# Performance work log

Hardware: AMD Instinct MI355X
Metric: run time of the kernel (lower is better)

## Reference

```python
import jax, jax.numpy as jnp
import numpy as np

D_MODEL = 1024
NUM_HEADS = 16
HEAD_DIM = D_MODEL // NUM_HEADS


def setup_inputs() -> dict:
    key = jax.random.key(0)
    ks = jax.random.split(key, 9)
    s = 1.0 / np.sqrt(D_MODEL)
    inp = {"x": jax.random.normal(ks[0], (2, 2048, D_MODEL), dtype=jnp.float32)}
    for i, name in enumerate(["q", "k", "v", "o"]):
        inp[f"W_{name}"] = jax.random.uniform(ks[1 + i], (D_MODEL, D_MODEL), dtype=jnp.float32, minval=-s, maxval=s)
        inp[f"b_{name}"] = jax.random.uniform(ks[5 + i], (D_MODEL,), dtype=jnp.float32, minval=-s, maxval=s)
    return inp


def reference(x, W_q, b_q, W_k, b_k, W_v, b_v, W_o, b_o):
    B, S, _ = x.shape
    def split_heads(t):  # [B,S,D] -> [B,H,S,Dh]
        return t.reshape(B, S, NUM_HEADS, HEAD_DIM).transpose(0, 2, 1, 3)
    q = split_heads(x @ W_q.T + b_q)
    k = split_heads(x @ W_k.T + b_k)
    v = split_heads(x @ W_v.T + b_v)
    scale = 1.0 / np.sqrt(HEAD_DIM).astype(np.float32)
    scores = jnp.einsum('bhqd,bhkd->bhqk', q, k) * scale  # [B,H,S,S]
    attn = jax.nn.softmax(scores, axis=-1)
    out = jnp.einsum('bhqk,bhkd->bhqd', attn, v)  # [B,H,S,Dh]
    out = out.transpose(0, 2, 1, 3).reshape(B, S, D_MODEL)
    return out @ W_o.T + b_o
```

## Files before the change

### kernel.cpp

```cpp
#include <hip/hip_runtime.h>
#include <hip/hip_bf16.h>

typedef __attribute__((ext_vector_type(8))) short short8;
typedef __attribute__((ext_vector_type(4))) float f32x4;
typedef __attribute__((ext_vector_type(16))) float f32x16;
typedef unsigned short ushort_t;
typedef unsigned int uint_t;

#define LOG2E 1.4426950408889634f

#if __has_builtin(__builtin_amdgcn_exp2f)
#define EXP2(x) __builtin_amdgcn_exp2f(x)
#else
#define EXP2(x) exp2f(x)
#endif

__device__ __forceinline__ ushort_t f2bf(float f) {
    union { float f; unsigned int i; } x; x.f = f;
    unsigned int r = x.i + 0x7FFF + ((x.i >> 16) & 1);
    return (ushort_t)(r >> 16);
}
__device__ __forceinline__ float bf2f(ushort_t u) {
    union { unsigned int i; float f; } x; x.i = ((unsigned int)u) << 16; return x.f;
}
__device__ __forceinline__ uint_t cvtpk(float lo, float hi) {
    uint_t r;
    asm("v_cvt_pk_bf16_f32 %0, %1, %2" : "=v"(r) : "v"(lo), "v"(hi));
    return r;
}

__device__ __forceinline__ void gll16(const void* g, void* l) {
    __builtin_amdgcn_global_load_lds((const __attribute__((address_space(1))) unsigned int*)g,
                                     (__attribute__((address_space(3))) unsigned int*)l,
                                     16, 0, 0);
}

__device__ __forceinline__ int xcd_lin() {
    int gx = gridDim.x;
    int n  = gx * gridDim.y;
    int lin = blockIdx.y * gx + blockIdx.x;
    int cpx = n >> 3;
    return (lin & 7) * cpx + (lin >> 3);
}

__global__ __launch_bounds__(256) void convert_kernel(
    const float* __restrict__ x,
    const float* __restrict__ Wq, const float* __restrict__ Wk,
    const float* __restrict__ Wv, const float* __restrict__ Wo,
    const float* __restrict__ bq, const float* __restrict__ bk, const float* __restrict__ bv,
    ushort_t* __restrict__ xb, ushort_t* __restrict__ wqkv,
    ushort_t* __restrict__ wob, float* __restrict__ bqkv)
{
    int idx = blockIdx.x * 256 + threadIdx.x;
    const float* src; ushort_t* dst; int off;
    if (idx < 1048576) { src = x; dst = xb; off = idx * 4; }
    else if (idx < 1835008) {
        int e = (idx - 1048576) * 4;
        int wi = e >> 20; off = e & 1048575;
        src = (wi == 0) ? Wq : ((wi == 1) ? Wk : Wv);
        dst = wqkv + ((size_t)wi << 20);
    } else { off = (idx - 1835008) * 4; src = Wo; dst = wob; }
    float4 v = *reinterpret_cast<const float4*>(src + off);
    ushort_t o0 = f2bf(v.x), o1 = f2bf(v.y), o2 = f2bf(v.z), o3 = f2bf(v.w);
    ushort_t* d = dst + off;
    d[0] = o0; d[1] = o1; d[2] = o2; d[3] = o3;
    if (idx < 768) {
        int wi = idx >> 8; int o4 = (idx & 255) * 4;
        const float* bsrc = (wi == 0) ? bq : ((wi == 1) ? bk : bv);
        *reinterpret_cast<float4*>(bqkv + wi * 1024 + o4) =
            *reinterpret_cast<const float4*>(bsrc + o4);
    }
}

template<int WRITE_BF16, int BN, int WRITE_VT>
__global__ __launch_bounds__(256) void gemm_nt(
    const ushort_t* __restrict__ A, const ushort_t* __restrict__ Bm,
    const float* __restrict__ bias, void* __restrict__ Cout,
    ushort_t* __restrict__ Vt,
    int M, int N, int K)
{
    constexpr int NT = BN / 32;
    __shared__ ushort_t As[2][128 * 32];
    __shared__ ushort_t Bs[2][BN * 32];

    const int tid  = threadIdx.x;
    const int lane = tid & 63;
    const int wv   = tid >> 6;

    const int sw = xcd_lin();
    const int bx = sw % gridDim.x;
    const int by = sw / gridDim.x;
    const int m0 = by * 128;
    const int n0 = bx * BN;

    const int wr   = wv >> 1, wc = wv & 1;
    const int g    = lane >> 4, c = lane & 15;

    f32x4 acc[4][NT] = {};

    const int srow = lane >> 2;
    const int scol = (lane & 3) * 8;
    const ushort_t* Ag = A  + (size_t)(m0 + wv * 32 + srow) * K + scol;
    const ushort_t* Bg = Bm + (size_t)(n0 + (BN == 128 ? wv * 32 : wv * 16) + srow) * K + scol;

    auto STAGE = [&](int b, int k0) {
        gll16(Ag + k0,          &As[b][(wv * 32) * 32]);
        gll16(Ag + 16 * K + k0, &As[b][(wv * 32 + 16) * 32]);
        if (BN == 128) {
            gll16(Bg + k0,          &Bs[b][(wv * 32) * 32]);
            gll16(Bg + 16 * K + k0, &Bs[b][(wv * 32 + 16) * 32]);
        } else {
            gll16(Bg + k0,          &Bs[b][(wv * 16) * 32]);
        }
    };

    STAGE(0, 0);
    int cur = 0;
    for (int k0 = 0; k0 < K; k0 += 32) {
        if (k0 + 32 < K) {
            STAGE(cur ^ 1, k0 + 32);
            if (BN == 128) asm volatile("s_waitcnt vmcnt(4)" ::: "memory");
            else           asm volatile("s_waitcnt vmcnt(3)" ::: "memory");
        } else {
            asm volatile("s_waitcnt vmcnt(0)" ::: "memory");
        }
        __builtin_amdgcn_sched_barrier(0);
        __builtin_amdgcn_s_barrier();
        __builtin_amdgcn_sched_barrier(0);

        short8 af[4], bf[NT];
        #pragma unroll
        for (int i = 0; i < 4; i++)
            af[i] = *reinterpret_cast<const short8*>(&As[cur][(wr * 64 + i * 16 + c) * 32 + g * 8]);
        #pragma unroll
        for (int j = 0; j < NT; j++)
            bf[j] = *reinterpret_cast<const short8*>(&Bs[cur][(wc * (BN / 2) + j * 16 + c) * 32 + g * 8]);
        #pragma unroll
        for (int i = 0; i < 4; i++)
            #pragma unroll
            for (int j = 0; j < NT; j++)
                acc[i][j] = __builtin_amdgcn_mfma_f32_16x16x32_bf16(af[i], bf[j], acc[i][j], 0, 0, 0);

        asm volatile("s_waitcnt lgkmcnt(0)" ::: "memory");
        __builtin_amdgcn_sched_barrier(0);
        __builtin_amdgcn_s_barrier();
        __builtin_amdgcn_sched_barrier(0);
        cur ^= 1;
    }

    #pragma unroll
    for (int i = 0; i < 4; i++) {
        int row = m0 + wr * 64 + i * 16 + 4 * g;
        #pragma unroll
        for (int j = 0; j < NT; j++) {
            int col = n0 + wc * (BN / 2) + j * 16 + c;
            float bv_ = bias[col];
            float v0 = acc[i][j][0] + bv_;
            float v1 = acc[i][j][1] + bv_;
            float v2 = acc[i][j][2] + bv_;
            float v3 = acc[i][j][3] + bv_;
            if (WRITE_VT && col >= 2048) {
                int dcol = col - 2048;
                int hv = dcol >> 6, dd = dcol & 63;
                int bb = row >> 11, ss = row & 2047;
                uint_t w0 = cvtpk(v0, v1);
                uint_t w1 = cvtpk(v2, v3);
                uint_t* vp = reinterpret_cast<uint_t*>(
                    Vt + (((size_t)(bb * 16 + hv) * 64 + dd) * 2048 + ss));
                vp[0] = w0; vp[1] = w1;
            } else if (WRITE_BF16) {
                ushort_t* cp = (ushort_t*)Cout;
                cp[(size_t)(row + 0) * N + col] = f2bf(v0);
                cp[(size_t)(row + 1) * N + col] = f2bf(v1);
                cp[(size_t)(row + 2) * N + col] = f2bf(v2);
                cp[(size_t)(row + 3) * N + col] = f2bf(v3);
            } else {
                float* cp = (float*)Cout;
                cp[(size_t)(row + 0) * N + col] = v0;
                cp[(size_t)(row + 1) * N + col] = v1;
                cp[(size_t)(row + 2) * N + col] = v2;
                cp[(size_t)(row + 3) * N + col] = v3;
            }
        }
    }
}

__global__ __launch_bounds__(512, 4) void attn_kernel(
    const ushort_t* __restrict__ qkv, const ushort_t* __restrict__ Vt,
    ushort_t* __restrict__ out)
{
    __shared__ ushort_t smem[32768];

    const int tid  = threadIdx.x;
    const int lane = tid & 63;
    const int wv   = tid >> 6;
    const int wvi  = wv & 3;
    const int g2   = wv >> 2;
    const int sw   = xcd_lin();
    const int qt   = sw & 15;
    const int bh   = sw >> 4;
    const int b = bh >> 4, h = bh & 15;
    const int c  = lane & 31;
    const int hh = lane >> 5;

    const int q0 = qt * 128 + wvi * 32;
    const size_t tokbase = (size_t)b * 2048;

    short8 qf[4];
    {
        const ushort_t* qg = qkv + (tokbase + q0 + c) * 3072 + h * 64 + hh * 8;
        #pragma unroll
        for (int s = 0; s < 4; s++) {
            short8 v = *reinterpret_cast<const short8*>(qg + s * 16);
            short8 o;
            #pragma unroll
            for (int e = 0; e < 8; e++)
                o[e] = (short)f2bf(bf2f((ushort_t)v[e]) * (0.125f * LOG2E));
            qf[s] = o;
        }
    }

    const int l8 = lane & 7;
    const int l3 = lane >> 3;
    const int kkA = (l3 & 3) + 8 * ((l3 >> 2) & 1);
    const ushort_t* kg0 = qkv + (tokbase + g2 * 1024 + wvi * 16 + kkA) * 3072
                              + 1024 + h * 64 + (l8 ^ l3) * 8;
    const ushort_t* vg0 = Vt + ((size_t)bh * 64 + wvi * 16 + l3) * 2048
                             + g2 * 1024 + (l8 ^ l3) * 8;

    f32x16 oacc[2] = {};
    f32x16 sc[2];
    float l0 = 0.f, l1 = 0.f, l2 = 0.f, l3s = 0.f;

    auto STAGE = [&](int bb, int kt) {
        char* Kd = (char*)smem + g2 * 32768 + bb * 16384 + wvi * 2048;
        char* Vd = Kd + 8192;
        const ushort_t* ks = kg0 + (size_t)(kt * 64) * 3072;
        gll16(ks,                     Kd);
        gll16(ks + (size_t)4 * 3072,  Kd + 1024);
        const ushort_t* vs = vg0 + kt * 64;
        gll16(vs,            Vd);
        gll16(vs + 8 * 2048, Vd + 1024);
    };

    STAGE(0, 0);
    int cur = 0;

    for (int it = 0; it < 16; it++) {
        if (it + 1 < 16) {
            STAGE(cur ^ 1, it + 1);
            asm volatile("s_waitcnt vmcnt(4)" ::: "memory");
        } else {
            asm volatile("s_waitcnt vmcnt(0)" ::: "memory");
        }
        __builtin_amdgcn_sched_barrier(0);
        __builtin_amdgcn_s_barrier();
        __builtin_amdgcn_sched_barrier(0);

        const char* KlB = (const char*)smem + g2 * 32768 + cur * 16384;
        const char* VlB = KlB + 8192;

        sc[0] = f32x16{}; sc[1] = f32x16{};
        __builtin_amdgcn_s_setprio(1);
        #pragma unroll
        for (int st = 0; st < 4; st++) {
            const int chB = (((2 * st + hh) ^ (c & 7)) << 4);
            short8 ak0 = *reinterpret_cast<const short8*>(KlB + (c     ) * 128 + chB);
            short8 ak1 = *reinterpret_cast<const short8*>(KlB + (32 + c) * 128 + chB);
            sc[0] = __builtin_amdgcn_mfma_f32_32x32x16_bf16(ak0, qf[st], sc[0], 0, 0, 0);
            sc[1] = __builtin_amdgcn_mfma_f32_32x32x16_bf16(ak1, qf[st], sc[1], 0, 0, 0);
        }
        __builtin_amdgcn_s_setprio(0);

        #pragma unroll
        for (int t = 0; t < 2; t++) {
            #pragma unroll
            for (int r = 0; r < 16; r += 4) {
                sc[t][r]   = EXP2(sc[t][r]);   l0  += sc[t][r];
                sc[t][r+1] = EXP2(sc[t][r+1]); l1  += sc[t][r+1];
                sc[t][r+2] = EXP2(sc[t][r+2]); l2  += sc[t][r+2];
                sc[t][r+3] = EXP2(sc[t][r+3]); l3s += sc[t][r+3];
            }
        }

        __builtin_amdgcn_s_setprio(1);
        #pragma unroll
        for (int s = 0; s < 4; s++) {
            const int t0 = s >> 1;
            const int rb = (s & 1) * 8;
            union { uint_t u[4]; short8 s8; } pu;
            pu.u[0] = cvtpk(sc[t0][rb + 0], sc[t0][rb + 1]);
            pu.u[1] = cvtpk(sc[t0][rb + 2], sc[t0][rb + 3]);
            pu.u[2] = cvtpk(sc[t0][rb + 4], sc[t0][rb + 5]);
            pu.u[3] = cvtpk(sc[t0][rb + 6], sc[t0][rb + 7]);

            const int chB = (((2 * s + hh) ^ (c & 7)) << 4);
            short8 av0 = *reinterpret_cast<const short8*>(VlB + (c     ) * 128 + chB);
            short8 av1 = *reinterpret_cast<const short8*>(VlB + (32 + c) * 128 + chB);
            oacc[0] = __builtin_amdgcn_mfma_f32_32x32x16_bf16(av0, pu.s8, oacc[0], 0, 0, 0);
            oacc[1] = __builtin_amdgcn_mfma_f32_32x32x16_bf16(av1, pu.s8, oacc[1], 0, 0, 0);
        }
        __builtin_amdgcn_s_setprio(0);

        asm volatile("s_waitcnt lgkmcnt(0)" ::: "memory");
        __builtin_amdgcn_sched_barrier(0);
        __builtin_amdgcn_s_barrier();
        __builtin_amdgcn_sched_barrier(0);
        cur ^= 1;
    }

    float l_own = (l0 + l1) + (l2 + l3s);
    float* dump = (float*)smem;
    const int di = (wvi * 64 + lane) * 34;
    if (g2) {
        #pragma unroll
        for (int r = 0; r < 16; r++) { dump[di + r] = oacc[0][r]; dump[di + 16 + r] = oacc[1][r]; }
        dump[di + 32] = l_own;
    }
    __syncthreads();
    if (!g2) {
        #pragma unroll
        for (int r = 0; r < 16; r++) { oacc[0][r] += dump[di + r]; oacc[1][r] += dump[di + 16 + r]; }
        l_own += dump[di + 32];
        float l_tot = l_own + __shfl_xor(l_own, 32);
        float invl = 1.0f / l_tot;

        ushort_t* Olw = (ushort_t*)((char*)smem + 36864 + wvi * 4608);
        #pragma unroll
        for (int td = 0; td < 2; td++)
            #pragma unroll
            for (int rr = 0; rr < 4; rr++)
                #pragma unroll
                for (int j2 = 0; j2 < 2; j2++) {
                    int r = 4 * rr + 2 * j2;
                    float v0 = (td == 0) ? oacc[0][r] : oacc[1][r];
                    float v1 = (td == 0) ? oacc[0][r + 1] : oacc[1][r + 1];
                    uint_t wd = cvtpk(v0 * invl, v1 * invl);
                    int dcol = 32 * td + 4 * hh + 8 * rr + 2 * j2;
                    *reinterpret_cast<uint_t*>(&Olw[c * 72 + dcol]) = wd;
                }
        int row = lane >> 1;
        int e0  = (lane & 1) * 32;
        ushort_t* og = out + (tokbase + q0 + row) * 1024 + h * 64 + e0;
        #pragma unroll
        for (int k2 = 0; k2 < 4; k2++) {
            short8 v;
            #pragma unroll
            for (int e = 0; e < 8; e++) v[e] = (short)Olw[row * 72 + e0 + k2 * 8 + e];
            *reinterpret_cast<short8*>(og + k2 * 8) = v;
        }
    }
}

extern "C" void kernel_launch(void* const* d_in, const int* in_sizes, int n_in,
                              void* d_out, int out_size, void* d_ws, size_t ws_size,
                              hipStream_t stream) {
    const float* x  = (const float*)d_in[0];
    const float* Wq = (const float*)d_in[1];
    const float* bq = (const float*)d_in[2];
    const float* Wk = (const float*)d_in[3];
    const float* bk = (const float*)d_in[4];
    const float* Wv = (const float*)d_in[5];
    const float* bv = (const float*)d_in[6];
    const float* Wo = (const float*)d_in[7];
    const float* bo = (const float*)d_in[8];

    uintptr_t w = (uintptr_t)d_ws;
    ushort_t* xb    = (ushort_t*)w;  w += 8388608;
    ushort_t* wqkv  = (ushort_t*)w;  w += 6291456;
    ushort_t* wob   = (ushort_t*)w;  w += 2097152;
    float*    bqkv  = (float*)w;     w += 12288;
    ushort_t* qkv   = (ushort_t*)w;  w += 25165824;
    ushort_t* attno = (ushort_t*)w;  w += 8388608;
    ushort_t* Vt    = (ushort_t*)w;  w += 8388608;

    convert_kernel<<<8192, 256, 0, stream>>>(x, Wq, Wk, Wv, Wo, bq, bk, bv,
                                             xb, wqkv, wob, bqkv);
    gemm_nt<1, 128, 1><<<dim3(24, 32), 256, 0, stream>>>(xb, wqkv, bqkv, qkv, Vt, 4096, 3072, 1024);
    attn_kernel<<<dim3(16, 32), 512, 0, stream>>>(qkv, Vt, attno);
    gemm_nt<0, 64, 0><<<dim3(16, 32), 256, 0, stream>>>(attno, wob, bo, (void*)d_out, nullptr, 4096, 1024, 1024);
}
```

Measured before the change: 107.6 us.

## Split attention KV range across four wave groups with 1024-thread blocks

The attention kernel now runs 16 waves per block instead of 8. The key/value sequence is split into four 512-token quarters, and each group streams 32-key tiles instead of 64-key tiles. Partial outputs and row sums from three of the groups are reduced into group zero through shared memory in two passes, separated by extra barriers. The aim is more latency hiding and parallelism per query tile, at the cost of more reduction traffic, more synchronisation, and smaller MFMA work per iteration.

```diff
diff --git a/kernel.cpp b/kernel.cpp
--- a/kernel.cpp
+++ b/kernel.cpp
@@ -185,7 +185,7 @@
     }
 }
 
-__global__ __launch_bounds__(512, 4) void attn_kernel(
+__global__ __launch_bounds__(1024, 8) void attn_kernel(
     const ushort_t* __restrict__ qkv, const ushort_t* __restrict__ Vt,
     ushort_t* __restrict__ out)
 {
@@ -194,8 +194,8 @@
     const int tid  = threadIdx.x;
     const int lane = tid & 63;
     const int wv   = tid >> 6;
-    const int wvi  = wv & 3;
-    const int g2   = wv >> 2;
+    const int wq   = wv & 3;
+    const int kq   = wv >> 2;
     const int sw   = xcd_lin();
     const int qt   = sw & 15;
     const int bh   = sw >> 4;
@@ -203,7 +203,7 @@
     const int c  = lane & 31;
     const int hh = lane >> 5;
 
-    const int q0 = qt * 128 + wvi * 32;
+    const int q0 = qt * 128 + wq * 32;
     const size_t tokbase = (size_t)b * 2048;
 
     short8 qf[4];
@@ -222,25 +222,22 @@
 
     const int l8 = lane & 7;
     const int l3 = lane >> 3;
-    const int kkA = (l3 & 3) + 8 * ((l3 >> 2) & 1);
-    const ushort_t* kg0 = qkv + (tokbase + g2 * 1024 + wvi * 16 + kkA) * 3072
-                              + 1024 + h * 64 + (l8 ^ l3) * 8;
-    const ushort_t* vg0 = Vt + ((size_t)bh * 64 + wvi * 16 + l3) * 2048
-                             + g2 * 1024 + (l8 ^ l3) * 8;
+    const int kkA = (l3 & 3) + 4 * (wq & 1) + 8 * ((l3 >> 2) & 1) + 16 * (wq >> 1);
+    const ushort_t* kg0 = qkv + (tokbase + kq * 512 + kkA) * 3072
+                              + 1024 + h * 64 + ((l8 ^ l3) * 8);
+    const int vrow = wq * 16 + ((lane >> 2) & 15);
+    const int vch  = (lane & 3) ^ ((lane >> 3) & 3);
+    const ushort_t* vg0 = Vt + ((size_t)bh * 64 + vrow) * 2048 + kq * 512 + vch * 8;
 
     f32x16 oacc[2] = {};
-    f32x16 sc[2];
-    float l0 = 0.f, l1 = 0.f, l2 = 0.f, l3s = 0.f;
+    f32x16 sc0;
+    float p0 = 0.f, p1 = 0.f, p2 = 0.f, p3 = 0.f;
 
     auto STAGE = [&](int bb, int kt) {
-        char* Kd = (char*)smem + g2 * 32768 + bb * 16384 + wvi * 2048;
-        char* Vd = Kd + 8192;
-        const ushort_t* ks = kg0 + (size_t)(kt * 64) * 3072;
-        gll16(ks,                     Kd);
-        gll16(ks + (size_t)4 * 3072,  Kd + 1024);
-        const ushort_t* vs = vg0 + kt * 64;
-        gll16(vs,            Vd);
-        gll16(vs + 8 * 2048, Vd + 1024);
+        char* Kd = (char*)smem + kq * 16384 + bb * 8192 + wq * 1024;
+        char* Vd = Kd + 4096;
+        gll16(kg0 + (size_t)(kt * 32) * 3072, Kd);
+        gll16(vg0 + kt * 32,                  Vd);
     };
 
     STAGE(0, 0);
@@ -249,7 +246,7 @@
     for (int it = 0; it < 16; it++) {
         if (it + 1 < 16) {
             STAGE(cur ^ 1, it + 1);
-            asm volatile("s_waitcnt vmcnt(4)" ::: "memory");
+            asm volatile("s_waitcnt vmcnt(2)" ::: "memory");
         } else {
             asm volatile("s_waitcnt vmcnt(0)" ::: "memory");
         }
@@ -257,46 +254,40 @@
         __builtin_amdgcn_s_barrier();
         __builtin_amdgcn_sched_barrier(0);
 
-        const char* KlB = (const char*)smem + g2 * 32768 + cur * 16384;
-        const char* VlB = KlB + 8192;
-
-        sc[0] = f32x16{}; sc[1] = f32x16{};
+        const char* KlB = (const char*)smem + kq * 16384 + cur * 8192;
+        const char* VlB = KlB + 4096;
+
+        sc0 = f32x16{};
         __builtin_amdgcn_s_setprio(1);
         #pragma unroll
         for (int st = 0; st < 4; st++) {
             const int chB = (((2 * st + hh) ^ (c & 7)) << 4);
-            short8 ak0 = *reinterpret_cast<const short8*>(KlB + (c     ) * 128 + chB);
-            short8 ak1 = *reinterpret_cast<const short8*>(KlB + (32 + c) * 128 + chB);
-            sc[0] = __builtin_amdgcn_mfma_f32_32x32x16_bf16(ak0, qf[st], sc[0], 0, 0, 0);
-            sc[1] = __builtin_amdgcn_mfma_f32_32x32x16_bf16(ak1, qf[st], sc[1], 0, 0, 0);
+            short8 ak = *reinterpret_cast<const short8*>(KlB + c * 128 + chB);
+            sc0 = __builtin_amdgcn_mfma_f32_32x32x16_bf16(ak, qf[st], sc0, 0, 0, 0);
         }
         __builtin_amdgcn_s_setprio(0);
 
         #pragma unroll
-        for (int t = 0; t < 2; t++) {
-            #pragma unroll
-            for (int r = 0; r < 16; r += 4) {
-                sc[t][r]   = EXP2(sc[t][r]);   l0  += sc[t][r];
-                sc[t][r+1] = EXP2(sc[t][r+1]); l1  += sc[t][r+1];
-                sc[t][r+2] = EXP2(sc[t][r+2]); l2  += sc[t][r+2];
-                sc[t][r+3] = EXP2(sc[t][r+3]); l3s += sc[t][r+3];
-            }
+        for (int r = 0; r < 16; r += 4) {
+            sc0[r]   = EXP2(sc0[r]);   p0 += sc0[r];
+            sc0[r+1] = EXP2(sc0[r+1]); p1 += sc0[r+1];
+            sc0[r+2] = EXP2(sc0[r+2]); p2 += sc0[r+2];
+            sc0[r+3] = EXP2(sc0[r+3]); p3 += sc0[r+3];
         }
 
         __builtin_amdgcn_s_setprio(1);
         #pragma unroll
-        for (int s = 0; s < 4; s++) {
-            const int t0 = s >> 1;
-            const int rb = (s & 1) * 8;
+        for (int s = 0; s < 2; s++) {
+            const int rb = s * 8;
             union { uint_t u[4]; short8 s8; } pu;
-            pu.u[0] = cvtpk(sc[t0][rb + 0], sc[t0][rb + 1]);
-            pu.u[1] = cvtpk(sc[t0][rb + 2], sc[t0][rb + 3]);
-            pu.u[2] = cvtpk(sc[t0][rb + 4], sc[t0][rb + 5]);
-            pu.u[3] = cvtpk(sc[t0][rb + 6], sc[t0][rb + 7]);
-
-            const int chB = (((2 * s + hh) ^ (c & 7)) << 4);
-            short8 av0 = *reinterpret_cast<const short8*>(VlB + (c     ) * 128 + chB);
-            short8 av1 = *reinterpret_cast<const short8*>(VlB + (32 + c) * 128 + chB);
+            pu.u[0] = cvtpk(sc0[rb + 0], sc0[rb + 1]);
+            pu.u[1] = cvtpk(sc0[rb + 2], sc0[rb + 3]);
+            pu.u[2] = cvtpk(sc0[rb + 4], sc0[rb + 5]);
+            pu.u[3] = cvtpk(sc0[rb + 6], sc0[rb + 7]);
+
+            const int chV = (((2 * s + hh) ^ ((c >> 1) & 3)) << 4);
+            short8 av0 = *reinterpret_cast<const short8*>(VlB + (c     ) * 64 + chV);
+            short8 av1 = *reinterpret_cast<const short8*>(VlB + (32 + c) * 64 + chV);
             oacc[0] = __builtin_amdgcn_mfma_f32_32x32x16_bf16(av0, pu.s8, oacc[0], 0, 0, 0);
             oacc[1] = __builtin_amdgcn_mfma_f32_32x32x16_bf16(av1, pu.s8, oacc[1], 0, 0, 0);
         }
@@ -309,23 +300,47 @@
         cur ^= 1;
     }
 
-    float l_own = (l0 + l1) + (l2 + l3s);
+    float l_own = (p0 + p1) + (p2 + p3);
     float* dump = (float*)smem;
-    const int di = (wvi * 64 + lane) * 34;
-    if (g2) {
-        #pragma unroll
-        for (int r = 0; r < 16; r++) { dump[di + r] = oacc[0][r]; dump[di + 16 + r] = oacc[1][r]; }
-        dump[di + 32] = l_own;
-    }
-    __syncthreads();
-    if (!g2) {
-        #pragma unroll
-        for (int r = 0; r < 16; r++) { oacc[0][r] += dump[di + r]; oacc[1][r] += dump[di + 16 + r]; }
-        l_own += dump[di + 32];
+    __syncthreads();
+    if (kq) {
+        int di = (((kq - 1) * 4 + wq) * 64 + lane) * 17;
+        #pragma unroll
+        for (int r = 0; r < 16; r++) dump[di + r] = oacc[0][r];
+        dump[di + 16] = l_own;
+    }
+    __syncthreads();
+    if (!kq) {
+        #pragma unroll
+        for (int src = 0; src < 3; src++) {
+            int di = ((src * 4 + wq) * 64 + lane) * 17;
+            #pragma unroll
+            for (int r = 0; r < 16; r++) oacc[0][r] += dump[di + r];
+            l_own += dump[di + 16];
+        }
+    }
+    __syncthreads();
+    if (kq) {
+        int di = (((kq - 1) * 4 + wq) * 64 + lane) * 17;
+        #pragma unroll
+        for (int r = 0; r < 16; r++) dump[di + r] = oacc[1][r];
+    }
+    __syncthreads();
+    if (!kq) {
+        #pragma unroll
+        for (int src = 0; src < 3; src++) {
+            int di = ((src * 4 + wq) * 64 + lane) * 17;
+            #pragma unroll
+            for (int r = 0; r < 16; r++) oacc[1][r] += dump[di + r];
+        }
+    }
+    __syncthreads();
+
+    if (!kq) {
         float l_tot = l_own + __shfl_xor(l_own, 32);
         float invl = 1.0f / l_tot;
 
-        ushort_t* Olw = (ushort_t*)((char*)smem + 36864 + wvi * 4608);
+        ushort_t* Olw = (ushort_t*)((char*)smem + wq * 4608);
         #pragma unroll
         for (int td = 0; td < 2; td++)
             #pragma unroll
@@ -377,6 +392,6 @@
     convert_kernel<<<8192, 256, 0, stream>>>(x, Wq, Wk, Wv, Wo, bq, bk, bv,
                                              xb, wqkv, wob, bqkv);
     gemm_nt<1, 128, 1><<<dim3(24, 32), 256, 0, stream>>>(xb, wqkv, bqkv, qkv, Vt, 4096, 3072, 1024);
-    attn_kernel<<<dim3(16, 32), 512, 0, stream>>>(qkv, Vt, attno);
+    attn_kernel<<<dim3(16, 32), 1024, 0, stream>>>(qkv, Vt, attno);
     gemm_nt<0, 64, 0><<<dim3(16, 32), 256, 0, stream>>>(attno, wob, bo, (void*)d_out, nullptr, 4096, 1024, 1024);
 }
```

Result: slower. 384.7 us (+257.4%).
